# Optimization experiments

Hardware: AMD Instinct MI355X
Metric: run time of the kernel (lower is better)

Reference implementation:

```python
import jax, jax.numpy as jnp
import numpy as np

F_SIZE = 8          # filter_size (even, >4 -> sinc mode)
C, H, W = 3, 720, 1280


def setup_inputs() -> dict:
    key = jax.random.key(0)
    k1, k2 = jax.random.split(key)
    x = jax.random.normal(k1, (1, C, H, W), dtype=jnp.float32)
    # optical flow in absolute pixels; a few pixels of motion is realistic
    flow = jax.random.normal(k2, (1, 2, H, W), dtype=jnp.float32) * 4.0
    return {"x": x, "flow": flow}


def _sinc_coeffs(s, offsets):
    # s: [H, W] fractional displacement in [0, 1); offsets: [F]
    # window * sinc interpolation coefficients -> [F, H, W]
    t = s[None, :, :] - offsets[:, None, None]
    return jnp.cos(jnp.pi * t / F_SIZE) * jnp.sinc(t)


def reference(x, flow):
    # Warper.forward in training mode (module default): q_flow = flow (no
    # fractional_accuracy rounding, which only applies in eval mode).
    _, C_, H_, W_ = x.shape
    fs = F_SIZE
    # neighbor tap offsets: -fs//2+1 .. fs//2  (e.g. -3..4 for fs=8)
    offsets = jnp.arange(-(fs // 2) + 1, fs // 2 + 1, dtype=jnp.float32)

    fx = flow[0, 0]  # horizontal (column) flow [H, W]
    fy = flow[0, 1]  # vertical (row) flow    [H, W]
    rfx = jnp.floor(fx)
    rfy = jnp.floor(fy)
    sx = fx - rfx    # fractional part in [0, 1)
    sy = fy - rfy

    col = jnp.arange(W_, dtype=jnp.float32)[None, :]   # [1, W]
    row = jnp.arange(H_, dtype=jnp.float32)[:, None]   # [H, 1]
    # integer neighbor coordinates, clamped (padding_mode='border') [F, H, W]
    ix = jnp.clip(col[None] + rfx[None] + offsets[:, None, None], 0, W_ - 1).astype(jnp.int32)
    iy = jnp.clip(row[None] + rfy[None] + offsets[:, None, None], 0, H_ - 1).astype(jnp.int32)

    x0 = x[0]  # [C, H, W]
    # multi-tap gather: [C, F_i, F_j, H, W] (nearest grid_sample of integer coords)
    gathered = x0[:, iy[:, None, :, :], ix[None, :, :, :]]

    cx = _sinc_coeffs(sx, offsets)  # [F, H, W] horizontal coefficients
    cy = _sinc_coeffs(sy, offsets)  # [F, H, W] vertical coefficients
    # separable interpolation: sum over j (columns) then i (rows), fused
    out = jnp.einsum('cijhw,jhw,ihw->chw', gathered, cx, cy)
    return out[None]  # [1, C, H, W]
```

## Files before the change

### kernel.cpp

```cpp
#include <hip/hip_runtime.h>
#include <math.h>

#define CC 3
#define HH 720
#define WW 1280
#define HW (HH * WW)

#define TW 64
#define TH 4
#define GX (WW / TW)
#define GY (HH / TH)
#define NWG (GX * GY)
#define NTHR 256

#define SW 1288
#define PLANE (HH * SW)
#define WS_HALFS (6 * PLANE + 8)
#define WS_BYTES ((size_t)WS_HALFS * 2)

#define RMAX 16
#define NBY (TH - 1 + 2 * RMAX + 1)
#define NKEY (NBY * 2 + 1)

typedef float f4 __attribute__((ext_vector_type(4), aligned(4)));
typedef _Float16 h8 __attribute__((ext_vector_type(8), aligned(4)));
typedef _Float16 h8a __attribute__((ext_vector_type(8), aligned(16)));
typedef _Float16 h2v __attribute__((ext_vector_type(2)));

#if __has_builtin(__builtin_amdgcn_fdot2)
#define HAVE_FDOT2 1
#endif

__constant__ float COSK[8] = {0.38268343f, 0.70710678f, 0.92387953f, 1.0f,
                              0.92387953f, 0.70710678f, 0.38268343f, 0.0f};
__constant__ float SINK[8] = {-0.92387953f, -0.70710678f, -0.38268343f, 0.0f,
                              0.38268343f, 0.70710678f, 0.92387953f, 1.0f};
__constant__ float SGNK[8] = {-1.0f, 1.0f, -1.0f, 1.0f, -1.0f, 1.0f, -1.0f, 1.0f};

__device__ __forceinline__ void sinc_weights(float s, float* wgt) {
    const float PI = 3.14159265358979f;
    float sp = __sinf(PI * s);
    float s8, c8;
    __sincosf(PI * s * 0.125f, &s8, &c8);
#pragma unroll
    for (int j = 0; j < 8; ++j) {
        float t = s - (float)(j - 3);
        float win = c8 * COSK[j] + s8 * SINK[j];
        float r = (t == 0.0f) ? 1.0f : __fdividef(sp * SGNK[j], PI * t);
        wgt[j] = win * r;
    }
}

__device__ __forceinline__ void sinc_weights_h2(float s, h2v* cwp) {
    const float PI = 3.14159265358979f;
    float sp = __sinf(PI * s);
    float s8, c8;
    __sincosf(PI * s * 0.125f, &s8, &c8);
#pragma unroll
    for (int jj = 0; jj < 4; ++jj) {
        float w0, w1;
        {
            int j = 2 * jj;
            float t = s - (float)(j - 3);
            float win = c8 * COSK[j] + s8 * SINK[j];
            float r = (t == 0.0f) ? 1.0f : __fdividef(sp * SGNK[j], PI * t);
            w0 = win * r;
        }
        {
            int j = 2 * jj + 1;
            float t = s - (float)(j - 3);
            float win = c8 * COSK[j] + s8 * SINK[j];
            float r = (t == 0.0f) ? 1.0f : __fdividef(sp * SGNK[j], PI * t);
            w1 = win * r;
        }
        cwp[jj] = (h2v){(_Float16)w0, (_Float16)w1};
    }
}

__device__ __forceinline__ float dot8f(h8 v, const h2v* cw) {
#ifdef HAVE_FDOT2
    h2v* p = (h2v*)&v;
    float a = __builtin_amdgcn_fdot2(p[0], cw[0], 0.0f, false);
    a = __builtin_amdgcn_fdot2(p[1], cw[1], a, false);
    a = __builtin_amdgcn_fdot2(p[2], cw[2], a, false);
    a = __builtin_amdgcn_fdot2(p[3], cw[3], a, false);
    return a;
#else
    float r = 0.f;
#pragma unroll
    for (int j = 0; j < 8; ++j)
        r = fmaf((float)v[j], (float)cw[j >> 1][j & 1], r);
    return r;
#endif
}

__global__ __launch_bounds__(256) void conv_kernel(const float* __restrict__ x,
                                                   _Float16* __restrict__ ws) {
    int tid = blockIdx.x * blockDim.x + threadIdx.x;
    if (tid >= CC * HH * (WW / 8)) return;
    int k8 = tid % (WW / 8);
    int rest = tid / (WW / 8);
    int k = k8 * 8;
    const float* src = x + rest * WW + k;
    f4 va = *(const f4*)src;
    f4 vb = *(const f4*)(src + 4);
    float xm1 = (k8 == 0) ? src[0] : src[-1];
    _Float16 m1 = (_Float16)xm1;
    _Float16 v0 = (_Float16)va.x, v1 = (_Float16)va.y,
             v2 = (_Float16)va.z, v3 = (_Float16)va.w;
    _Float16 v4 = (_Float16)vb.x, v5 = (_Float16)vb.y,
             v6 = (_Float16)vb.z, v7 = (_Float16)vb.w;
    int dstA = rest * SW + k;
    *(h8a*)(ws + dstA) = (h8a){v0, v1, v2, v3, v4, v5, v6, v7};
    int dstB = 3 * PLANE + rest * SW + k;
    *(h8a*)(ws + dstB) = (h8a){m1, v0, v1, v2, v3, v4, v5, v6};
}

__device__ __forceinline__ void pixel_slow(const float* __restrict__ x,
                                           int bx, int by,
                                           const float* cxw, const float* cyw,
                                           float& r0, float& r1, float& r2) {
    int xcl[8];
#pragma unroll
    for (int j = 0; j < 8; ++j) xcl[j] = min(max(bx + (j - 3), 0), WW - 1);
    r0 = 0.f; r1 = 0.f; r2 = 0.f;
#pragma unroll
    for (int i = 0; i < 8; ++i) {
        int o = min(max(by + (i - 3), 0), HH - 1) * WW;
        float cyi = cyw[i];
        const float* p0 = x + o;
        const float* p1 = p0 + HW;
        const float* p2 = p1 + HW;
        float rs0 = 0.f, rs1 = 0.f, rs2 = 0.f;
#pragma unroll
        for (int j = 0; j < 8; ++j) {
            float cj = cxw[j];
            rs0 = fmaf(p0[xcl[j]], cj, rs0);
            rs1 = fmaf(p1[xcl[j]], cj, rs1);
            rs2 = fmaf(p2[xcl[j]], cj, rs2);
        }
        r0 = fmaf(cyi, rs0, r0);
        r1 = fmaf(cyi, rs1, r1);
        r2 = fmaf(cyi, rs2, r2);
    }
}

__global__ __launch_bounds__(NTHR) void warp_kernel(const float* __restrict__ x,
                                                    const float* __restrict__ flow,
                                                    const _Float16* __restrict__ hx,
                                                    float* __restrict__ out) {
    __shared__ float sfx[NTHR], sfy[NTHR];
    __shared__ unsigned short sid[NTHR];
    __shared__ int HIST[128], CUR[128];

    int tid = threadIdx.x;

    int bid = blockIdx.x;
    int swz = (bid & 7) * (NWG / 8) + (bid >> 3);
    int tx = swz % GX;
    int ty = swz / GX;
    int w0 = tx * TW;
    int h0 = ty * TH;

    if (tid < 128) HIST[tid] = 0;

    int w = w0 + (tid & 63);
    int h = h0 + (tid >> 6);
    int idx = h * WW + w;
    float fx = flow[idx];
    float fy = flow[HW + idx];
    sfx[tid] = fx;
    sfy[tid] = fy;
    __syncthreads();

    int key;
    {
        int ix = (int)floorf(fx), iy = (int)floorf(fy);
        int s = w + ix - 3;
        int by = h + iy;
        bool fast = (iy >= -RMAX) && (iy <= RMAX) && (s >= 0) && (s <= WW - 8);
        key = fast ? ((by - (h0 - RMAX)) * 2 + (s & 1)) : (NKEY - 1);
    }
    atomicAdd(&HIST[key], 1);
    __syncthreads();

    if (tid < 64) {
        int a = HIST[2 * tid], b = HIST[2 * tid + 1];
        int sum = a + b;
#pragma unroll
        for (int d = 1; d < 64; d <<= 1) {
            int vv = __shfl_up(sum, d, 64);
            if (tid >= d) sum += vv;
        }
        int excl = sum - a - b;
        CUR[2 * tid] = excl;
        CUR[2 * tid + 1] = excl + a;
    }
    __syncthreads();

    {
        int pos = atomicAdd(&CUR[key], 1);
        sid[pos] = (unsigned short)tid;
    }
    __syncthreads();

    int me = sid[tid];
    float mfx = sfx[me], mfy = sfy[me];
    int mw = w0 + (me & 63);
    int mh = h0 + (me >> 6);
    float rfx = floorf(mfx), rfy = floorf(mfy);
    float sx = mfx - rfx, sy = mfy - rfy;
    int ix = (int)rfx, iy = (int)rfy;
    int s = mw + ix - 3;
    int by = mh + iy;
    bool fast = (iy >= -RMAX) && (iy <= RMAX) && (s >= 0) && (s <= WW - 8);

    float r0, r1, r2;
    if (fast) {
        int ro[8];
#pragma unroll
        for (int i = 0; i < 8; ++i)
            ro[i] = min(max(by + (i - 3), 0), HH - 1) * SW;
        const _Float16* hp = hx + ((s & 1) ? (3 * PLANE + 1) : 0) + s;

        h2v cwp[4];
        sinc_weights_h2(sx, cwp);
        float cyw[8];
        sinc_weights(sy, cyw);

        r0 = r1 = r2 = 0.f;
#pragma unroll
        for (int i = 0; i < 8; ++i) {
            h8 v0 = *(const h8*)(hp + ro[i]);
            h8 v1 = *(const h8*)(hp + ro[i] + PLANE);
            h8 v2 = *(const h8*)(hp + ro[i] + 2 * PLANE);
            float cyi = cyw[i];
            r0 = fmaf(cyi, dot8f(v0, cwp), r0);
            r1 = fmaf(cyi, dot8f(v1, cwp), r1);
            r2 = fmaf(cyi, dot8f(v2, cwp), r2);
        }
    } else {
        float cxw[8], cyw[8];
        sinc_weights(sx, cxw);
        sinc_weights(sy, cyw);
        pixel_slow(x, mw + ix, mh + iy, cxw, cyw, r0, r1, r2);
    }

    int oidx = mh * WW + mw;
    out[oidx] = r0;
    out[HW + oidx] = r1;
    out[2 * HW + oidx] = r2;
}

__global__ __launch_bounds__(256) void warp_kernel_f32(const float* __restrict__ x,
                                                       const float* __restrict__ flow,
                                                       float* __restrict__ out) {
    int idx = blockIdx.x * blockDim.x + threadIdx.x;
    if (idx >= HW) return;
    int w = idx % WW;
    int h = idx / WW;
    float fx = flow[idx], fy = flow[HW + idx];
    float rfx = floorf(fx), rfy = floorf(fy);
    int bx = w + (int)rfx, by = h + (int)rfy;
    float cxw[8], cyw[8];
    sinc_weights(fx - rfx, cxw);
    sinc_weights(fy - rfy, cyw);
    float r0, r1, r2;
    pixel_slow(x, bx, by, cxw, cyw, r0, r1, r2);
    out[idx] = r0;
    out[HW + idx] = r1;
    out[2 * HW + idx] = r2;
}

extern "C" void kernel_launch(void* const* d_in, const int* in_sizes, int n_in,
                              void* d_out, int out_size, void* d_ws, size_t ws_size,
                              hipStream_t stream) {
    const float* x = (const float*)d_in[0];
    const float* flow = (const float*)d_in[1];
    float* out = (float*)d_out;

    if (ws_size >= WS_BYTES) {
        _Float16* ws = (_Float16*)d_ws;
        int nconv = CC * HH * (WW / 8);
        conv_kernel<<<(nconv + 255) / 256, 256, 0, stream>>>(x, ws);
        warp_kernel<<<NWG, NTHR, 0, stream>>>(x, flow, ws, out);
    } else {
        warp_kernel_f32<<<(HW + 255) / 256, 256, 0, stream>>>(x, flow, out);
    }
}
```

Baseline: 48.49 us.

## Split each fast-path pixel's 8 row taps across 8 lanes with shuffle reduction

Fast-path pixels now write their coefficients and metadata to shared memory. Each pixel is then processed by a group of 8 lanes, one tap row per lane, and the partial sums are combined with xor shuffles. Results are staged in shared memory so the final global stores are coalesced in original pixel order. The aim is to raise memory-level parallelism and give the gather loads a more coherent access pattern. In exchange it adds shared-memory traffic, two extra barriers, a shuffle reduction, and lanes left idle when the fast count is not a multiple of 8.

Measured after the change: 62.84 us. +29.6%, slower.

```diff
diff --git a/kernel.cpp b/kernel.cpp
--- a/kernel.cpp
+++ b/kernel.cpp
@@ -23,6 +23,7 @@
 #define NKEY (NBY * 2 + 1)
 
 typedef float f4 __attribute__((ext_vector_type(4), aligned(4)));
+typedef float f4a __attribute__((ext_vector_type(4), aligned(16)));
 typedef _Float16 h8 __attribute__((ext_vector_type(8), aligned(4)));
 typedef _Float16 h8a __attribute__((ext_vector_type(8), aligned(16)));
 typedef _Float16 h2v __attribute__((ext_vector_type(2)));
@@ -30,6 +31,8 @@
 #if __has_builtin(__builtin_amdgcn_fdot2)
 #define HAVE_FDOT2 1
 #endif
+
+union CW { h2v h[4]; uint4 u; };
 
 __constant__ float COSK[8] = {0.38268343f, 0.70710678f, 0.92387953f, 1.0f,
                               0.92387953f, 0.70710678f, 0.38268343f, 0.0f};
@@ -152,6 +155,11 @@
     __shared__ float sfx[NTHR], sfy[NTHR];
     __shared__ unsigned short sid[NTHR];
     __shared__ int HIST[128], CUR[128];
+    __shared__ uint4 scw[NTHR];
+    __shared__ __align__(16) float scy[NTHR * 8];
+    __shared__ int smeta[NTHR];
+    __shared__ float res2s[NTHR];
+    __shared__ int SF;
 
     int tid = threadIdx.x;
 
@@ -195,6 +203,7 @@
         int excl = sum - a - b;
         CUR[2 * tid] = excl;
         CUR[2 * tid + 1] = excl + a;
+        if (tid == (NKEY - 1) / 2) SF = excl;
     }
     __syncthreads();
 
@@ -204,52 +213,84 @@
     }
     __syncthreads();
 
-    int me = sid[tid];
-    float mfx = sfx[me], mfy = sfy[me];
-    int mw = w0 + (me & 63);
-    int mh = h0 + (me >> 6);
-    float rfx = floorf(mfx), rfy = floorf(mfy);
-    float sx = mfx - rfx, sy = mfy - rfy;
-    int ix = (int)rfx, iy = (int)rfy;
-    int s = mw + ix - 3;
-    int by = mh + iy;
-    bool fast = (iy >= -RMAX) && (iy <= RMAX) && (s >= 0) && (s <= WW - 8);
-
-    float r0, r1, r2;
-    if (fast) {
-        int ro[8];
-#pragma unroll
-        for (int i = 0; i < 8; ++i)
-            ro[i] = min(max(by + (i - 3), 0), HH - 1) * SW;
-        const _Float16* hp = hx + ((s & 1) ? (3 * PLANE + 1) : 0) + s;
-
-        h2v cwp[4];
-        sinc_weights_h2(sx, cwp);
-        float cyw[8];
-        sinc_weights(sy, cyw);
-
-        r0 = r1 = r2 = 0.f;
-#pragma unroll
-        for (int i = 0; i < 8; ++i) {
-            h8 v0 = *(const h8*)(hp + ro[i]);
-            h8 v1 = *(const h8*)(hp + ro[i] + PLANE);
-            h8 v2 = *(const h8*)(hp + ro[i] + 2 * PLANE);
-            float cyi = cyw[i];
-            r0 = fmaf(cyi, dot8f(v0, cwp), r0);
-            r1 = fmaf(cyi, dot8f(v1, cwp), r1);
-            r2 = fmaf(cyi, dot8f(v2, cwp), r2);
-        }
-    } else {
-        float cxw[8], cyw[8];
-        sinc_weights(sx, cxw);
-        sinc_weights(sy, cyw);
-        pixel_slow(x, mw + ix, mh + iy, cxw, cyw, r0, r1, r2);
-    }
-
-    int oidx = mh * WW + mw;
-    out[oidx] = r0;
-    out[HW + oidx] = r1;
-    out[2 * HW + oidx] = r2;
+    {
+        int me = sid[tid];
+        float mfx = sfx[me], mfy = sfy[me];
+        int mw = w0 + (me & 63);
+        int mh = h0 + (me >> 6);
+        float rfx = floorf(mfx), rfy = floorf(mfy);
+        float sx = mfx - rfx, sy = mfy - rfy;
+        int ix = (int)rfx, iy = (int)rfy;
+        int s = mw + ix - 3;
+        int by = mh + iy;
+        bool fast = (iy >= -RMAX) && (iy <= RMAX) && (s >= 0) && (s <= WW - 8);
+        if (fast) {
+            CW cwu;
+            sinc_weights_h2(sx, cwu.h);
+            scw[tid] = cwu.u;
+            float cyw[8];
+            sinc_weights(sy, cyw);
+            f4a* pcy = (f4a*)&scy[tid * 8];
+            pcy[0] = (f4a){cyw[0], cyw[1], cyw[2], cyw[3]};
+            pcy[1] = (f4a){cyw[4], cyw[5], cyw[6], cyw[7]};
+            smeta[tid] = (s << 16) | (by & 0xFFFF);
+        } else {
+            float cxw[8], cyw[8];
+            sinc_weights(sx, cxw);
+            sinc_weights(sy, cyw);
+            float r0, r1, r2;
+            pixel_slow(x, mw + ix, mh + iy, cxw, cyw, r0, r1, r2);
+            sfx[me] = r0;
+            sfy[me] = r1;
+            res2s[me] = r2;
+        }
+    }
+    __syncthreads();
+
+    {
+        int F = SF;
+        int wv = tid >> 6;
+        int ln = tid & 63;
+        int grp = ln >> 3;
+        int ri = ln & 7;
+        for (int t = 0; t < 8; ++t) {
+            int pi = wv * 64 + t * 8 + grp;
+            if (pi < F) {
+                int m = smeta[pi];
+                int s2 = m >> 16;
+                int by2 = (short)(m & 0xFFFF);
+                int row = min(max(by2 + ri - 3, 0), HH - 1);
+                const _Float16* hp =
+                    hx + ((s2 & 1) ? (3 * PLANE + 1) : 0) + s2 + row * SW;
+                h8 v0 = *(const h8*)(hp);
+                h8 v1 = *(const h8*)(hp + PLANE);
+                h8 v2 = *(const h8*)(hp + 2 * PLANE);
+                CW cwu;
+                cwu.u = scw[pi];
+                float cyi = scy[pi * 8 + ri];
+                float p0 = cyi * dot8f(v0, cwu.h);
+                float p1 = cyi * dot8f(v1, cwu.h);
+                float p2 = cyi * dot8f(v2, cwu.h);
+#pragma unroll
+                for (int d = 1; d < 8; d <<= 1) {
+                    p0 += __shfl_xor(p0, d, 64);
+                    p1 += __shfl_xor(p1, d, 64);
+                    p2 += __shfl_xor(p2, d, 64);
+                }
+                if (ri == 0) {
+                    int me2 = sid[pi];
+                    sfx[me2] = p0;
+                    sfy[me2] = p1;
+                    res2s[me2] = p2;
+                }
+            }
+        }
+    }
+    __syncthreads();
+
+    out[idx] = sfx[tid];
+    out[HW + idx] = sfy[tid];
+    out[2 * HW + idx] = res2s[tid];
 }
 
 __global__ __launch_bounds__(256) void warp_kernel_f32(const float* __restrict__ x,
```
